# Performance work log

Hardware: AMD Instinct MI355X
Metric: run time of the kernel (lower is better)

## Reference

```python
import jax, jax.numpy as jnp
from jax import lax
import numpy as np

B, N, C, M = 4, 20000, 512, 1024  # batch, points, seed_feat_dim, M_POINT
GRASPNESS_THRESHOLD = 0.1


def setup_inputs() -> dict:
    key = jax.random.key(0)
    k1, k2, k3, k4 = jax.random.split(key, 4)
    return {
        "point_clouds": jax.random.uniform(k1, (B, N, 3), jnp.float32),
        "seed_features": jax.random.normal(k2, (B, C, N), jnp.float32),
        "objectness_score": jax.random.normal(k3, (B, 2, N), jnp.float32),
        "graspness_score": jax.random.normal(k4, (B, N), jnp.float32),
    }


def _fps(xyz, mask, m):
    """Furthest point sampling restricted to masked-valid points.
    xyz: (n,3), mask: (n,) bool. Returns (m,) int indices.
    Matches compacted-array FPS: first pick = first valid point."""
    n = xyz.shape[0]
    first = jnp.argmax(mask)
    mind0 = jnp.full((n,), jnp.inf, xyz.dtype)

    def step(carry, _):
        mind, last = carry
        d = jnp.sum((xyz - xyz[last]) ** 2, axis=-1)
        mind = jnp.minimum(mind, d)
        nxt = jnp.argmax(jnp.where(mask, mind, -jnp.inf))
        return (mind, nxt), last

    _, idx = lax.scan(step, (mind0, first), None, length=m)
    return idx


def reference(point_clouds, seed_features, objectness_score, graspness_score):
    # graspable mask: objectness argmax == 1 AND graspness > threshold
    obj_mask = jnp.argmax(objectness_score, axis=1) == 1            # (B,N)
    grasp_mask = graspness_score > GRASPNESS_THRESHOLD              # (B,N)
    mask = obj_mask & grasp_mask

    # masked FPS per batch element (original loops over B)
    fps_idx = jax.vmap(_fps, in_axes=(0, 0, None))(point_clouds, mask, M)  # (B,M)
    xyz_g = jnp.take_along_axis(point_clouds, fps_idx[:, :, None], axis=1)  # (B,M,3)

    # three_nn: 3 nearest neighbors of each sampled point in the full cloud
    d2 = jnp.sum((xyz_g[:, :, None, :] - point_clouds[:, None, :, :]) ** 2, axis=-1)  # (B,M,N)
    neg_d2, idx3 = lax.top_k(-d2, 3)                                # (B,M,3)
    dist = jnp.sqrt(jnp.maximum(-neg_d2, 0.0))
    w = 1.0 / (dist + 1e-8)
    w = w / jnp.sum(w, axis=-1, keepdims=True)                      # (B,M,3)

    # three_interpolate: inverse-distance-weighted gather of features
    feats_n = seed_features.transpose(0, 2, 1)                      # (B,N,C)
    nb = jax.vmap(lambda f, i: f[i])(feats_n, idx3)                 # (B,M,3,C)
    interp = jnp.einsum("bmkc,bmk->bcm", nb, w)                   # (B,C,M)
    return interp
```

## Files before the change

kernel.cpp:

```cpp
#include <hip/hip_runtime.h>
#include <cstdint>

#define BB 4
#define NN 20000
#define CC 512
#define MM 1024
#define GTHR 0.1f
#define FPS_T 512
#define LDSCAP 5120
#define QB 8

#define INFF __builtin_huge_valf()
typedef unsigned long long u64;

__device__ __forceinline__ float wave_max_f32(float v) {
  int i = __float_as_int(v);
  i = __builtin_amdgcn_update_dpp(i, i, 0x121, 0xF, 0xF, false);
  v = fmaxf(v, __int_as_float(i));
  i = __float_as_int(v);
  i = __builtin_amdgcn_update_dpp(i, i, 0x122, 0xF, 0xF, false);
  v = fmaxf(v, __int_as_float(i));
  i = __float_as_int(v);
  i = __builtin_amdgcn_update_dpp(i, i, 0x124, 0xF, 0xF, false);
  v = fmaxf(v, __int_as_float(i));
  i = __float_as_int(v);
  i = __builtin_amdgcn_update_dpp(i, i, 0x128, 0xF, 0xF, false);
  v = fmaxf(v, __int_as_float(i));
  v = fmaxf(v, __int_as_float(
                   __builtin_amdgcn_ds_swizzle(__float_as_int(v), 0x401F)));
  v = fmaxf(v, __shfl_xor(v, 32));
  return v;
}

__device__ __forceinline__ unsigned merge8(const u64* pkrow) {
  const ulonglong2* p2 = (const ulonglong2*)pkrow;
  ulonglong2 e0 = p2[0], e1 = p2[1], e2 = p2[2], e3 = p2[3];
  u64 a = e0.x > e0.y ? e0.x : e0.y;
  u64 b = e1.x > e1.y ? e1.x : e1.y;
  u64 c = e2.x > e2.y ? e2.x : e2.y;
  u64 d = e3.x > e3.y ? e3.x : e3.y;
  a = a > b ? a : b;
  c = c > d ? c : d;
  a = a > c ? a : c;
  return ~(unsigned)(a & 0xffffffffull);
}

template <int K>
__device__ void fps_lds(int nv_, const float2* lxy, const float* lz,
                        float4* fpsXyzb, u64 (*pk)[8]) {
  const int t = threadIdx.x;
  const int lane = t & 63, w = t >> 6;
  float x[K], y[K], z[K], mind[K];
#pragma unroll
  for (int s = 0; s < K; ++s) {
    int j = s * FPS_T + t;
    if (j < nv_) {
      float2 p = lxy[j];
      x[s] = p.x; y[s] = p.y; z[s] = lz[j]; mind[s] = INFF;
    } else {
      x[s] = 0.f; y[s] = 0.f; z[s] = 0.f; mind[s] = 0.f;
    }
  }
  float2 q0 = lxy[0];
  float qx = q0.x, qy = q0.y, qz = lz[0];
  if (t == 0) fpsXyzb[0] = make_float4(qx, qy, qz, 0.f);
  int buf = 0;
  for (int r = 1; r < MM; ++r) {
    float bm;
#pragma unroll
    for (int s = 0; s < K; ++s) {
      float dx = x[s] - qx, dy = y[s] - qy, dz = z[s] - qz;
      float d = fmaf(dz, dz, fmaf(dy, dy, dx * dx));
      float m = fminf(mind[s], d);
      mind[s] = m;
      bm = (s == 0) ? m : fmaxf(bm, m);
    }
    bm = wave_max_f32(bm);
    unsigned jw = 0u;
    bool found = false;
#pragma unroll
    for (int s = 0; s < K; ++s) {
      if (!found) {
        u64 bal = __ballot(mind[s] == bm);
        if (bal) {
          jw = (unsigned)(s * FPS_T + (w << 6)) +
               (unsigned)__builtin_ctzll(bal);
          found = true;
        }
      }
    }
    if (lane == 0)
      pk[buf][w] = ((u64)__float_as_uint(bm) << 32) | (unsigned)~jw;
    __syncthreads();
    unsigned jg = merge8(&pk[buf][0]);
    float2 qq = lxy[jg];
    qx = qq.x; qy = qq.y; qz = lz[jg];
    if (t == 0) fpsXyzb[r] = make_float4(qx, qy, qz, 0.f);
    buf ^= 1;
  }
}

__device__ void fps_fallback(int nv_, const float4* cxg, float4* fpsXyzb,
                             float* mindg, u64 (*pk)[8]) {
  const int t = threadIdx.x;
  const int lane = t & 63, w = t >> 6;
  for (int j = t; j < nv_; j += FPS_T) mindg[j] = INFF;
  __syncthreads();
  float4 q = cxg[0];
  float qx = q.x, qy = q.y, qz = q.z;
  if (t == 0) fpsXyzb[0] = make_float4(qx, qy, qz, 0.f);
  int buf = 0;
  const int kmax = (nv_ + FPS_T - 1) / FPS_T;
  for (int r = 1; r < MM; ++r) {
    float bm = 0.f;
    for (int j = t; j < nv_; j += FPS_T) {
      float4 p = cxg[j];
      float dx = p.x - qx, dy = p.y - qy, dz = p.z - qz;
      float d = fmaf(dz, dz, fmaf(dy, dy, dx * dx));
      float m = fminf(mindg[j], d);
      mindg[j] = m;
      bm = fmaxf(bm, m);
    }
    bm = wave_max_f32(bm);
    unsigned jw = 0u;
    bool found = false;
    for (int k = 0; k < kmax && !found; ++k) {
      int j = k * FPS_T + t;
      bool match = (j < nv_) && (mindg[j] == bm);
      u64 bal = __ballot(match);
      if (bal) {
        jw = (unsigned)(k * FPS_T + (w << 6)) + (unsigned)__builtin_ctzll(bal);
        found = true;
      }
    }
    if (lane == 0)
      pk[buf][w] = ((u64)__float_as_uint(bm) << 32) | (unsigned)~jw;
    __syncthreads();
    unsigned jg = merge8(&pk[buf][0]);
    float4 qq = cxg[jg];
    qx = qq.x; qy = qq.y; qz = qq.z;
    if (t == 0) fpsXyzb[r] = make_float4(qx, qy, qz, 0.f);
    buf ^= 1;
  }
}

__global__ __launch_bounds__(FPS_T) void fps_kernel(
    const float* __restrict__ pc, const float* __restrict__ obj,
    const float* __restrict__ grasp, float4* __restrict__ fpsXyz,
    float4* __restrict__ cxyz_g, float* __restrict__ mindg) {
  __shared__ float2 lxy[LDSCAP];
  __shared__ float lz[LDSCAP];
  __shared__ alignas(16) u64 pk[2][8];
  __shared__ int wtot[8];
  const int b = blockIdx.x;
  const int t = threadIdx.x;
  const int lane = t & 63, w = t >> 6;
  const float* pcb = pc + (size_t)b * NN * 3;
  const float* o0 = obj + (size_t)b * 2 * NN;
  const float* o1 = o0 + NN;
  const float* gb = grasp + (size_t)b * NN;
  float4* fpsXyzb = fpsXyz + (size_t)b * MM;
  float4* cxg = cxyz_g + (size_t)b * NN;

  const int SPAN = 2500;
  const int wstart = w * SPAN;
  u64 vmask = 0;
  int cnt = 0;
#pragma unroll
  for (int g = 0; g < 40; ++g) {
    int off = g * 64 + lane;
    bool v = false;
    if (off < SPAN) {
      int i = wstart + off;
      v = (o1[i] > o0[i]) && (gb[i] > GTHR);
    }
    u64 bal = __ballot(v);
    if (v) vmask |= (1ull << g);
    cnt += (int)__popcll(bal);
  }
  if (lane == 0) wtot[w] = cnt;
  __syncthreads();
  int base = 0, nv_ = 0;
#pragma unroll
  for (int k = 0; k < 8; ++k) {
    int c = wtot[k];
    if (k < w) base += c;
    nv_ += c;
  }
  const bool useg = (nv_ > LDSCAP);
#pragma unroll
  for (int g = 0; g < 40; ++g) {
    bool v = (vmask >> g) & 1ull;
    u64 bal = __ballot(v);
    if (v) {
      int i = wstart + g * 64 + lane;
      float xx = pcb[3 * i], yy = pcb[3 * i + 1], zz = pcb[3 * i + 2];
      int pos = base + (int)__popcll(bal & ((1ull << lane) - 1ull));
      if (pos < LDSCAP) { lxy[pos] = make_float2(xx, yy); lz[pos] = zz; }
      if (useg) cxg[pos] = make_float4(xx, yy, zz, 0.f);
    }
    base += (int)__popcll(bal);
  }
  __syncthreads();

  if (nv_ == 0) {
    float4 p0 = make_float4(pcb[0], pcb[1], pcb[2], 0.f);
    for (int r = t; r < MM; r += FPS_T) fpsXyzb[r] = p0;
    return;
  }
  int slots = (nv_ + FPS_T - 1) / FPS_T;
  if (slots <= 3)       fps_lds<3>(nv_, lxy, lz, fpsXyzb, pk);
  else if (slots <= 6)  fps_lds<6>(nv_, lxy, lz, fpsXyzb, pk);
  else if (slots <= 9)  fps_lds<9>(nv_, lxy, lz, fpsXyzb, pk);
  else if (slots <= 10) fps_lds<10>(nv_, lxy, lz, fpsXyzb, pk);
  else fps_fallback(nv_, cxg, fpsXyzb, mindg + (size_t)b * NN, pk);
}

__device__ __forceinline__ bool nn_before(float ad, int ai, float bd, int bi) {
  return (ad < bd) || (ad == bd && ai < bi);
}

__device__ __forceinline__ void merge3(float* ad, int* ai,
                                       float b0, float b1, float b2,
                                       int j0, int j1, int j2) {
  bool c0 = nn_before(ad[0], ai[0], b0, j0);
  float r0d = c0 ? ad[0] : b0; int r0i = c0 ? ai[0] : j0;
  float Xd = c0 ? b0 : ad[0];  int Xi = c0 ? j0 : ai[0];
  bool c1 = nn_before(ad[1], ai[1], b1, j1);
  float Yd = c1 ? ad[1] : b1;  int Yi = c1 ? ai[1] : j1;
  bool c2 = nn_before(Xd, Xi, Yd, Yi);
  float r1d = c2 ? Xd : Yd;    int r1i = c2 ? Xi : Yi;
  float Wd = c2 ? Yd : Xd;     int Wi = c2 ? Yi : Xi;
  bool c3 = nn_before(ad[2], ai[2], b2, j2);
  float Vd = c3 ? ad[2] : b2;  int Vi = c3 ? ai[2] : j2;
  bool c4 = nn_before(Wd, Wi, Vd, Vi);
  float r2d = c4 ? Wd : Vd;    int r2i = c4 ? Wi : Vi;
  ad[0] = r0d; ad[1] = r1d; ad[2] = r2d;
  ai[0] = r0i; ai[1] = r1i; ai[2] = r2i;
}

__global__ void three_nn_kernel(const float* __restrict__ pc,
                                const float4* __restrict__ fpsXyz,
                                int* __restrict__ idx3,
                                float* __restrict__ w3) {
  const int blk = blockIdx.x;
  const int b = blk / (MM / QB);
  const int qbase = (blk % (MM / QB)) * QB;
  const int t = threadIdx.x;
  const int lane = t & 63, w = t >> 6;
  const float* pcb = pc + (size_t)b * NN * 3;
  float qx[QB], qy[QB], qz[QB];
#pragma unroll
  for (int qq = 0; qq < QB; ++qq) {
    float4 p = fpsXyz[(size_t)b * MM + qbase + qq];
    qx[qq] = p.x; qy[qq] = p.y; qz[qq] = p.z;
  }
  float qd[QB][3]; int qi[QB][3];
#pragma unroll
  for (int qq = 0; qq < QB; ++qq)
#pragma unroll
    for (int k = 0; k < 3; ++k) { qd[qq][k] = INFF; qi[qq][k] = 0x7fffffff; }

  const int nchunk = (NN + 255) / 256;
  for (int c = 0; c < nchunk; ++c) {
    int i = c * 256 + t;
    if (i < NN) {
      float pxx = pcb[3 * i], pyy = pcb[3 * i + 1], pzz = pcb[3 * i + 2];
#pragma unroll
      for (int qq = 0; qq < QB; ++qq) {
        float dx = pxx - qx[qq], dy = pyy - qy[qq], dz = pzz - qz[qq];
        float d = fmaf(dz, dz, fmaf(dy, dy, dx * dx));
        if (d < qd[qq][2]) {
          bool lt0 = d < qd[qq][0], lt1 = d < qd[qq][1];
          qd[qq][2] = lt1 ? qd[qq][1] : d;  qi[qq][2] = lt1 ? qi[qq][1] : i;
          float nd1 = lt0 ? qd[qq][0] : (lt1 ? d : qd[qq][1]);
          int   ni1 = lt0 ? qi[qq][0] : (lt1 ? i : qi[qq][1]);
          qd[qq][1] = nd1; qi[qq][1] = ni1;
          qd[qq][0] = lt0 ? d : qd[qq][0];  qi[qq][0] = lt0 ? i : qi[qq][0];
        }
      }
    }
  }
#pragma unroll
  for (int off = 32; off; off >>= 1) {
#pragma unroll
    for (int qq = 0; qq < QB; ++qq) {
      float bd0 = __shfl_xor(qd[qq][0], off);
      float bd1 = __shfl_xor(qd[qq][1], off);
      float bd2 = __shfl_xor(qd[qq][2], off);
      int bi0 = __shfl_xor(qi[qq][0], off);
      int bi1 = __shfl_xor(qi[qq][1], off);
      int bi2 = __shfl_xor(qi[qq][2], off);
      merge3(qd[qq], qi[qq], bd0, bd1, bd2, bi0, bi1, bi2);
    }
  }
  __shared__ float smd[4][QB][3];
  __shared__ int smi[4][QB][3];
  if (lane == 0) {
#pragma unroll
    for (int qq = 0; qq < QB; ++qq)
#pragma unroll
      for (int k = 0; k < 3; ++k) { smd[w][qq][k] = qd[qq][k]; smi[w][qq][k] = qi[qq][k]; }
  }
  __syncthreads();
  if (t < QB) {
    int qq = t;
    float fd[3]; int fi[3];
#pragma unroll
    for (int k = 0; k < 3; ++k) { fd[k] = smd[0][qq][k]; fi[k] = smi[0][qq][k]; }
#pragma unroll
    for (int ww = 1; ww < 4; ++ww)
      merge3(fd, fi, smd[ww][qq][0], smd[ww][qq][1], smd[ww][qq][2],
             smi[ww][qq][0], smi[ww][qq][1], smi[ww][qq][2]);
    float wa = 1.f / (sqrtf(fmaxf(fd[0], 0.f)) + 1e-8f);
    float wb = 1.f / (sqrtf(fmaxf(fd[1], 0.f)) + 1e-8f);
    float wc = 1.f / (sqrtf(fmaxf(fd[2], 0.f)) + 1e-8f);
    float s = wa + wb + wc;
    size_t base3 = ((size_t)b * MM + qbase + qq) * 3;
    w3[base3] = wa / s; w3[base3 + 1] = wb / s; w3[base3 + 2] = wc / s;
    idx3[base3] = fi[0]; idx3[base3 + 1] = fi[1]; idx3[base3 + 2] = fi[2];
  }
}

__global__ void interp_kernel(const float* __restrict__ seed,
                              const int* __restrict__ idx3,
                              const float* __restrict__ w3,
                              float* __restrict__ out) {
  const int blk = blockIdx.x;
  const int b = blk / CC;
  const int c = blk % CC;
  const float* row = seed + ((size_t)b * CC + c) * NN;
  const int t = threadIdx.x;
#pragma unroll
  for (int u = 0; u < MM / 256; ++u) {
    int m = u * 256 + t;
    size_t base3 = ((size_t)b * MM + m) * 3;
    int i0 = idx3[base3], i1 = idx3[base3 + 1], i2 = idx3[base3 + 2];
    float w0 = w3[base3], w1 = w3[base3 + 1], w2 = w3[base3 + 2];
    float v = fmaf(w2, row[i2], fmaf(w1, row[i1], w0 * row[i0]));
    out[((size_t)b * CC + c) * MM + m] = v;
  }
}

extern "C" void kernel_launch(void* const* d_in, const int* in_sizes, int n_in,
                              void* d_out, int out_size, void* d_ws,
                              size_t ws_size, hipStream_t stream) {
  (void)in_sizes; (void)n_in; (void)out_size; (void)ws_size;
  const float* pc = (const float*)d_in[0];
  const float* seed = (const float*)d_in[1];
  const float* obj = (const float*)d_in[2];
  const float* grasp = (const float*)d_in[3];
  float* out = (float*)d_out;

  char* p = (char*)d_ws;
  float4* cxyz = (float4*)p;   p += sizeof(float4) * BB * NN;
  float4* fpsXyz = (float4*)p; p += sizeof(float4) * BB * MM;
  int* idx3 = (int*)p;         p += sizeof(int) * BB * MM * 3;
  float* w3 = (float*)p;       p += sizeof(float) * BB * MM * 3;
  float* mindg = (float*)p;    p += sizeof(float) * BB * NN;

  hipLaunchKernelGGL(fps_kernel, dim3(BB), dim3(FPS_T), 0, stream,
                     pc, obj, grasp, fpsXyz, cxyz, mindg);
  hipLaunchKernelGGL(three_nn_kernel, dim3(BB * MM / QB), dim3(256), 0, stream,
                     pc, fpsXyz, idx3, w3);
  hipLaunchKernelGGL(interp_kernel, dim3(BB * CC), dim3(256), 0, stream,
                     seed, idx3, w3, out);
}
```

Measured before the change: 1.262 ms.

## Double FPS block to 1024 threads and fuse argmax into packed wave reduction

Raises the FPS block from 512 to 1024 threads so each thread holds fewer candidate points, and retunes the per-wave span and K template choices to match. Each thread now tracks its own best index, and a 64-bit key (distance, inverted index) is reduced across the wave with DPP. This replaces the separate float max followed by a ballot search, and the merge across 16 waves picks the winner. Sampled points are written once at the end, one per thread, instead of by thread 0 every iteration. The trade-off is a wider 64-bit reduction and twice as many waves taking part in each block barrier.

```diff
diff --git a/kernel.cpp b/kernel.cpp
--- a/kernel.cpp
+++ b/kernel.cpp
@@ -6,48 +6,69 @@
 #define CC 512
 #define MM 1024
 #define GTHR 0.1f
-#define FPS_T 512
+#define FPS_T 1024
+#define NW (FPS_T / 64)
 #define LDSCAP 5120
 #define QB 8
 
 #define INFF __builtin_huge_valf()
 typedef unsigned long long u64;
 
-__device__ __forceinline__ float wave_max_f32(float v) {
-  int i = __float_as_int(v);
-  i = __builtin_amdgcn_update_dpp(i, i, 0x121, 0xF, 0xF, false);
-  v = fmaxf(v, __int_as_float(i));
-  i = __float_as_int(v);
-  i = __builtin_amdgcn_update_dpp(i, i, 0x122, 0xF, 0xF, false);
-  v = fmaxf(v, __int_as_float(i));
-  i = __float_as_int(v);
-  i = __builtin_amdgcn_update_dpp(i, i, 0x124, 0xF, 0xF, false);
-  v = fmaxf(v, __int_as_float(i));
-  i = __float_as_int(v);
-  i = __builtin_amdgcn_update_dpp(i, i, 0x128, 0xF, 0xF, false);
-  v = fmaxf(v, __int_as_float(i));
-  v = fmaxf(v, __int_as_float(
-                   __builtin_amdgcn_ds_swizzle(__float_as_int(v), 0x401F)));
-  v = fmaxf(v, __shfl_xor(v, 32));
-  return v;
-}
-
-__device__ __forceinline__ unsigned merge8(const u64* pkrow) {
+#define DPP_MAX_STEP(CTRL)                                                  \
+  {                                                                         \
+    unsigned lo = (unsigned)k, hi = (unsigned)(k >> 32);                    \
+    int ol = __builtin_amdgcn_update_dpp((int)lo, (int)lo, CTRL, 0xF, 0xF,  \
+                                         false);                            \
+    int oh = __builtin_amdgcn_update_dpp((int)hi, (int)hi, CTRL, 0xF, 0xF,  \
+                                         false);                            \
+    u64 o = ((u64)(unsigned)oh << 32) | (unsigned)ol;                       \
+    k = o > k ? o : k;                                                      \
+  }
+
+__device__ __forceinline__ u64 wave_max_u64(u64 k) {
+  DPP_MAX_STEP(0x121)
+  DPP_MAX_STEP(0x122)
+  DPP_MAX_STEP(0x124)
+  DPP_MAX_STEP(0x128)
+  {
+    unsigned lo = (unsigned)k, hi = (unsigned)(k >> 32);
+    int ol = __builtin_amdgcn_ds_swizzle((int)lo, 0x401F);
+    int oh = __builtin_amdgcn_ds_swizzle((int)hi, 0x401F);
+    u64 o = ((u64)(unsigned)oh << 32) | (unsigned)ol;
+    k = o > k ? o : k;
+  }
+  {
+    u64 o = __shfl_xor(k, 32);
+    k = o > k ? o : k;
+  }
+  return k;
+}
+
+__device__ __forceinline__ unsigned merge16(const u64* pkrow) {
   const ulonglong2* p2 = (const ulonglong2*)pkrow;
   ulonglong2 e0 = p2[0], e1 = p2[1], e2 = p2[2], e3 = p2[3];
+  ulonglong2 e4 = p2[4], e5 = p2[5], e6 = p2[6], e7 = p2[7];
   u64 a = e0.x > e0.y ? e0.x : e0.y;
   u64 b = e1.x > e1.y ? e1.x : e1.y;
   u64 c = e2.x > e2.y ? e2.x : e2.y;
   u64 d = e3.x > e3.y ? e3.x : e3.y;
+  u64 e = e4.x > e4.y ? e4.x : e4.y;
+  u64 f = e5.x > e5.y ? e5.x : e5.y;
+  u64 g = e6.x > e6.y ? e6.x : e6.y;
+  u64 h = e7.x > e7.y ? e7.x : e7.y;
   a = a > b ? a : b;
   c = c > d ? c : d;
+  e = e > f ? e : f;
+  g = g > h ? g : h;
   a = a > c ? a : c;
+  e = e > g ? e : g;
+  a = a > e ? a : e;
   return ~(unsigned)(a & 0xffffffffull);
 }
 
 template <int K>
 __device__ void fps_lds(int nv_, const float2* lxy, const float* lz,
-                        float4* fpsXyzb, u64 (*pk)[8]) {
+                        float4* fpsXyzb, u64 (*pk)[NW]) {
   const int t = threadIdx.x;
   const int lane = t & 63, w = t >> 6;
   float x[K], y[K], z[K], mind[K];
@@ -61,87 +82,72 @@
       x[s] = 0.f; y[s] = 0.f; z[s] = 0.f; mind[s] = 0.f;
     }
   }
-  float2 q0 = lxy[0];
-  float qx = q0.x, qy = q0.y, qz = lz[0];
-  if (t == 0) fpsXyzb[0] = make_float4(qx, qy, qz, 0.f);
+  float qx = lxy[0].x, qy = lxy[0].y, qz = lz[0];
+  unsigned jsave = 0;
   int buf = 0;
   for (int r = 1; r < MM; ++r) {
-    float bm;
+    float bm = -1.f;
+    int bs = 0;
 #pragma unroll
     for (int s = 0; s < K; ++s) {
       float dx = x[s] - qx, dy = y[s] - qy, dz = z[s] - qz;
       float d = fmaf(dz, dz, fmaf(dy, dy, dx * dx));
       float m = fminf(mind[s], d);
       mind[s] = m;
-      bm = (s == 0) ? m : fmaxf(bm, m);
-    }
-    bm = wave_max_f32(bm);
-    unsigned jw = 0u;
-    bool found = false;
-#pragma unroll
-    for (int s = 0; s < K; ++s) {
-      if (!found) {
-        u64 bal = __ballot(mind[s] == bm);
-        if (bal) {
-          jw = (unsigned)(s * FPS_T + (w << 6)) +
-               (unsigned)__builtin_ctzll(bal);
-          found = true;
-        }
-      }
-    }
-    if (lane == 0)
-      pk[buf][w] = ((u64)__float_as_uint(bm) << 32) | (unsigned)~jw;
+      bool better = m > bm;
+      bm = better ? m : bm;
+      bs = better ? s : bs;
+    }
+    unsigned j = (unsigned)(bs * FPS_T + t);
+    u64 key = ((u64)__float_as_uint(bm) << 32) | (unsigned)(~j);
+    key = wave_max_u64(key);
+    if (lane == 0) pk[buf][w] = key;
     __syncthreads();
-    unsigned jg = merge8(&pk[buf][0]);
+    unsigned jg = merge16(&pk[buf][0]);
     float2 qq = lxy[jg];
     qx = qq.x; qy = qq.y; qz = lz[jg];
-    if (t == 0) fpsXyzb[r] = make_float4(qx, qy, qz, 0.f);
+    if (r == (unsigned)t) jsave = jg;
     buf ^= 1;
   }
+  float2 pp = lxy[jsave];
+  fpsXyzb[t] = make_float4(pp.x, pp.y, lz[jsave], 0.f);
 }
 
 __device__ void fps_fallback(int nv_, const float4* cxg, float4* fpsXyzb,
-                             float* mindg, u64 (*pk)[8]) {
+                             float* mindg, u64 (*pk)[NW]) {
   const int t = threadIdx.x;
   const int lane = t & 63, w = t >> 6;
   for (int j = t; j < nv_; j += FPS_T) mindg[j] = INFF;
   __syncthreads();
   float4 q = cxg[0];
   float qx = q.x, qy = q.y, qz = q.z;
-  if (t == 0) fpsXyzb[0] = make_float4(qx, qy, qz, 0.f);
+  unsigned jsave = 0;
   int buf = 0;
-  const int kmax = (nv_ + FPS_T - 1) / FPS_T;
   for (int r = 1; r < MM; ++r) {
-    float bm = 0.f;
+    float bm = -1.f;
+    int bj = 0x7fffffff;
     for (int j = t; j < nv_; j += FPS_T) {
       float4 p = cxg[j];
       float dx = p.x - qx, dy = p.y - qy, dz = p.z - qz;
       float d = fmaf(dz, dz, fmaf(dy, dy, dx * dx));
       float m = fminf(mindg[j], d);
       mindg[j] = m;
-      bm = fmaxf(bm, m);
-    }
-    bm = wave_max_f32(bm);
-    unsigned jw = 0u;
-    bool found = false;
-    for (int k = 0; k < kmax && !found; ++k) {
-      int j = k * FPS_T + t;
-      bool match = (j < nv_) && (mindg[j] == bm);
-      u64 bal = __ballot(match);
-      if (bal) {
-        jw = (unsigned)(k * FPS_T + (w << 6)) + (unsigned)__builtin_ctzll(bal);
-        found = true;
-      }
-    }
-    if (lane == 0)
-      pk[buf][w] = ((u64)__float_as_uint(bm) << 32) | (unsigned)~jw;
+      bool better = m > bm;
+      bm = better ? m : bm;
+      bj = better ? j : bj;
+    }
+    u64 key = ((u64)__float_as_uint(bm) << 32) | (unsigned)(~(unsigned)bj);
+    key = wave_max_u64(key);
+    if (lane == 0) pk[buf][w] = key;
     __syncthreads();
-    unsigned jg = merge8(&pk[buf][0]);
+    unsigned jg = merge16(&pk[buf][0]);
     float4 qq = cxg[jg];
     qx = qq.x; qy = qq.y; qz = qq.z;
-    if (t == 0) fpsXyzb[r] = make_float4(qx, qy, qz, 0.f);
+    if (r == (unsigned)t) jsave = jg;
     buf ^= 1;
   }
+  float4 pp = cxg[jsave];
+  fpsXyzb[t] = pp;
 }
 
 __global__ __launch_bounds__(FPS_T) void fps_kernel(
@@ -150,8 +156,8 @@
     float4* __restrict__ cxyz_g, float* __restrict__ mindg) {
   __shared__ float2 lxy[LDSCAP];
   __shared__ float lz[LDSCAP];
-  __shared__ alignas(16) u64 pk[2][8];
-  __shared__ int wtot[8];
+  __shared__ alignas(16) u64 pk[2][NW];
+  __shared__ int wtot[NW];
   const int b = blockIdx.x;
   const int t = threadIdx.x;
   const int lane = t & 63, w = t >> 6;
@@ -162,12 +168,12 @@
   float4* fpsXyzb = fpsXyz + (size_t)b * MM;
   float4* cxg = cxyz_g + (size_t)b * NN;
 
-  const int SPAN = 2500;
+  const int SPAN = 1250;
   const int wstart = w * SPAN;
-  u64 vmask = 0;
+  unsigned vmask = 0;
   int cnt = 0;
 #pragma unroll
-  for (int g = 0; g < 40; ++g) {
+  for (int g = 0; g < 20; ++g) {
     int off = g * 64 + lane;
     bool v = false;
     if (off < SPAN) {
@@ -175,22 +181,22 @@
       v = (o1[i] > o0[i]) && (gb[i] > GTHR);
     }
     u64 bal = __ballot(v);
-    if (v) vmask |= (1ull << g);
+    if (v) vmask |= (1u << g);
     cnt += (int)__popcll(bal);
   }
   if (lane == 0) wtot[w] = cnt;
   __syncthreads();
   int base = 0, nv_ = 0;
 #pragma unroll
-  for (int k = 0; k < 8; ++k) {
+  for (int k = 0; k < NW; ++k) {
     int c = wtot[k];
     if (k < w) base += c;
     nv_ += c;
   }
   const bool useg = (nv_ > LDSCAP);
 #pragma unroll
-  for (int g = 0; g < 40; ++g) {
-    bool v = (vmask >> g) & 1ull;
+  for (int g = 0; g < 20; ++g) {
+    bool v = (vmask >> g) & 1u;
     u64 bal = __ballot(v);
     if (v) {
       int i = wstart + g * 64 + lane;
@@ -209,10 +215,10 @@
     return;
   }
   int slots = (nv_ + FPS_T - 1) / FPS_T;
-  if (slots <= 3)       fps_lds<3>(nv_, lxy, lz, fpsXyzb, pk);
-  else if (slots <= 6)  fps_lds<6>(nv_, lxy, lz, fpsXyzb, pk);
-  else if (slots <= 9)  fps_lds<9>(nv_, lxy, lz, fpsXyzb, pk);
-  else if (slots <= 10) fps_lds<10>(nv_, lxy, lz, fpsXyzb, pk);
+  if (slots <= 2)      fps_lds<2>(nv_, lxy, lz, fpsXyzb, pk);
+  else if (slots <= 3) fps_lds<3>(nv_, lxy, lz, fpsXyzb, pk);
+  else if (slots <= 4) fps_lds<4>(nv_, lxy, lz, fpsXyzb, pk);
+  else if (slots <= 5) fps_lds<5>(nv_, lxy, lz, fpsXyzb, pk);
   else fps_fallback(nv_, cxg, fpsXyzb, mindg + (size_t)b * NN, pk);
 }
 
```

New measurement: 1.681 ms. 1.33x slower.
